# Performance work log

Hardware: AMD Instinct MI355X
Metric: run time of the kernel (lower is better)

The kernel has to match this reference:

```python
import jax, jax.numpy as jnp
import numpy as np
import math

N_HEADS = 16
D_MODEL = 1024
DK = D_MODEL // N_HEADS
B, S = 2, 2048


def setup_inputs() -> dict:
    key = jax.random.key(0)
    ks = jax.random.split(key, 11)
    scale_in = 1.0 / math.sqrt(D_MODEL)
    scale_o = 1.0 / math.sqrt(N_HEADS * DK)
    return {
        "query": jax.random.normal(ks[0], (B, S, D_MODEL), jnp.float32),
        "key": jax.random.normal(ks[1], (B, S, D_MODEL), jnp.float32),
        "value": jax.random.normal(ks[2], (B, S, D_MODEL), jnp.float32),
        # stacked per-head projection weights [H, d_model, dk], biases [H, dk]
        "Wq": jax.random.normal(ks[3], (N_HEADS, D_MODEL, DK), jnp.float32) * scale_in,
        "bq": jax.random.normal(ks[4], (N_HEADS, DK), jnp.float32) * scale_in,
        "Wk": jax.random.normal(ks[5], (N_HEADS, D_MODEL, DK), jnp.float32) * scale_in,
        "bk": jax.random.normal(ks[6], (N_HEADS, DK), jnp.float32) * scale_in,
        "Wv": jax.random.normal(ks[7], (N_HEADS, D_MODEL, DK), jnp.float32) * scale_in,
        "bv": jax.random.normal(ks[8], (N_HEADS, DK), jnp.float32) * scale_in,
        "Wo": jax.random.normal(ks[9], (N_HEADS * DK, D_MODEL), jnp.float32) * scale_o,
        "bo": jax.random.normal(ks[10], (D_MODEL,), jnp.float32) * scale_o,
    }


def reference(query, key, value, Wq, bq, Wk, bk, Wv, bv, Wo, bo):
    # Per-head linear projections, vectorized over heads: [B,H,S,dk]
    q = jnp.einsum("bsd,hdk->bhsk", query, Wq) + bq[None, :, None, :]
    k = jnp.einsum("bsd,hdk->bhsk", key, Wk) + bk[None, :, None, :]
    v = jnp.einsum("bsd,hdk->bhsk", value, Wv) + bv[None, :, None, :]
    # Scaled dot-product scores [B,H,S,S]
    scores = jnp.einsum("bhsk,bhtk->bhst", q, k) / jnp.sqrt(jnp.asarray(DK, q.dtype))
    # FAITHFUL to source: nn.Softmax(dim=0) -> softmax over the BATCH axis
    attn = jax.nn.softmax(scores, axis=0)
    out = jnp.einsum("bhst,bhtk->bhsk", attn, v)  # [B,H,S,dk]
    # concat heads along feature dim (torch.cat dim=2)
    concat = out.transpose(0, 2, 1, 3).reshape(query.shape[0], query.shape[1], N_HEADS * DK)
    return concat @ Wo + bo
```

## Files before the change

kernel.cpp:

```cpp
#include <hip/hip_runtime.h>
#include <hip/hip_bf16.h>

#define B_ 2
#define S_ 2048
#define D_ 1024
#define H_ 16
#define DK_ 64
#define BS_ (B_ * S_)

typedef unsigned int u32;
typedef unsigned short u16;
typedef __attribute__((ext_vector_type(8))) short bf16x8;
typedef __attribute__((ext_vector_type(4))) float f32x4;

typedef const __attribute__((address_space(1))) void glb_cv;
typedef __attribute__((address_space(3))) void lds_v;

__device__ __forceinline__ void async_cp16(const void* g, void* l) {
    __builtin_amdgcn_global_load_lds((glb_cv*)g, (lds_v*)l, 16, 0, 0);
}

__device__ __forceinline__ float bf2f(u16 v) {
    union { u32 u; float f; } c; c.u = ((u32)v) << 16; return c.f;
}
__device__ __forceinline__ u16 f2bf(float f) {
    union { float f; u32 u; } c; c.f = f;
    u32 u = c.u;
    return (u16)((u + 0x7fffu + ((u >> 16) & 1u)) >> 16);
}
__device__ __forceinline__ u32 pack2(float a, float b) {
    return (u32)f2bf(a) | ((u32)f2bf(b) << 16);
}
__device__ __forceinline__ u32 packtr(float lo, float hi) {
    union { float f; u32 u; } a, b; a.f = lo; b.f = hi;
    return __builtin_amdgcn_perm(b.u, a.u, 0x07060302u);
}
__device__ __forceinline__ int sw64(int r, int c8) { return (((c8) + (r)) & 7) * 8; }

struct PrepArgs {
    const float* W[4]; u16* WT[4];
    const float* X[3]; u16* XB[3];
};
__global__ __launch_bounds__(256) void prep(PrepArgs a)
{
    const int id = blockIdx.x;
    const int tid = threadIdx.x;
    if (id >= 1024) {
        const int cid = id - 1024;
        const int z = cid >> 11;
        const size_t base = (size_t)(cid & 2047) * 2048 + tid * 8;
        const float* X = a.X[z];
        float4 x0 = *(const float4*)(X + base);
        float4 x1 = *(const float4*)(X + base + 4);
        uint4 o;
        o.x = pack2(x0.x, x0.y); o.y = pack2(x0.z, x0.w);
        o.z = pack2(x1.x, x1.y); o.w = pack2(x1.z, x1.w);
        *(uint4*)(a.XB[z] + base) = o;
        return;
    }
    __shared__ __attribute__((aligned(16))) u16 T[64][72];
    const int z = id >> 8;
    const int rem = id & 255;
    const float* W = a.W[z];
    u16* WT = a.WT[z];
    const int headMode = (z < 3) ? 1 : 0;
    const int k0 = (rem >> 4) * 64;
    const int n0 = (rem & 15) * 64;
    const int kr = tid >> 4;
    const int n4 = (tid & 15) * 4;
    #pragma unroll
    for (int pass = 0; pass < 4; ++pass) {
        int kk = k0 + pass * 16 + kr;
        const float* p = headMode
            ? (W + (size_t)((n0 + n4) >> 6) * (1024 * 64) + kk * 64 + ((n0 + n4) & 63))
            : (W + (size_t)kk * 1024 + n0 + n4);
        float4 v = *(const float4*)p;
        int krel = pass * 16 + kr;
        T[n4 + 0][krel] = f2bf(v.x);
        T[n4 + 1][krel] = f2bf(v.y);
        T[n4 + 2][krel] = f2bf(v.z);
        T[n4 + 3][krel] = f2bf(v.w);
    }
    __syncthreads();
    const int nr = tid >> 2;
    const int kq = (tid & 3) * 16;
    uint4 o0 = *(const uint4*)&T[nr][kq];
    uint4 o1 = *(const uint4*)&T[nr][kq + 8];
    u16* q = WT + (size_t)(n0 + nr) * 1024 + k0 + kq;
    *(uint4*)q = o0;
    *(uint4*)(q + 8) = o1;
}

struct ProjArgs {
    const u16* X[3];
    const u16* W[3];
    const float* bias[3];
    u16* Y[3];
};
__global__ __launch_bounds__(256) void proj3(ProjArgs pa)
{
    __shared__ __attribute__((aligned(16))) u16 As[2][128][32];
    __shared__ __attribute__((aligned(16))) u16 Bs[2][128][32];
    const int z = blockIdx.z;
    const u16* X = pa.X[z];
    const u16* WT = pa.W[z];
    const float* bias = pa.bias[z];
    u16* Y = pa.Y[z];
    const int neg = (z == 1);

    const int tid = threadIdx.x;
    const int lane = tid & 63;
    const int wave = tid >> 6;
    const int quad = lane >> 4;
    const int l16 = lane & 15;
    const int m0 = blockIdx.x * 128;
    const int n0 = blockIdx.y * 128;
    const int wm = (wave & 1) * 64, wn = (wave >> 1) * 64;

    f32x4 acc[4][4] = {};

    for (int k0 = 0; k0 < 1024; k0 += 64) {
        __syncthreads();
        #pragma unroll
        for (int ks = 0; ks < 2; ++ks)
            #pragma unroll
            for (int call = 0; call < 2; ++call) {
                const int c = tid + call * 256;
                const int row = c >> 2, cc = (c & 3) * 8;
                char* la = (char*)&As[ks][0][0] + (size_t)(c & ~63) * 16;
                async_cp16(X + (size_t)(m0 + row) * 1024 + k0 + ks * 32 + cc, la);
                char* lb = (char*)&Bs[ks][0][0] + (size_t)(c & ~63) * 16;
                async_cp16(WT + (size_t)(n0 + row) * 1024 + k0 + ks * 32 + cc, lb);
            }
        __syncthreads();

        #pragma unroll
        for (int ks = 0; ks < 2; ++ks) {
            bf16x8 af[4], bfr[4];
            #pragma unroll
            for (int mt = 0; mt < 4; ++mt)
                af[mt] = *(const bf16x8*)&As[ks][wm + mt * 16 + l16][quad * 8];
            #pragma unroll
            for (int nt = 0; nt < 4; ++nt)
                bfr[nt] = *(const bf16x8*)&Bs[ks][wn + nt * 16 + l16][quad * 8];
            #pragma unroll
            for (int mt = 0; mt < 4; ++mt)
                #pragma unroll
                for (int nt = 0; nt < 4; ++nt)
                    acc[mt][nt] = __builtin_amdgcn_mfma_f32_16x16x32_bf16(
                        af[mt], bfr[nt], acc[mt][nt], 0, 0, 0);
        }
    }

    if (z == 2) {
        #pragma unroll
        for (int nt = 0; nt < 4; ++nt) {
            const int col = n0 + wn + nt * 16 + l16;
            const float bv = bias[col];
            u16* vrow = Y + ((size_t)(col >> 6) * 64 + (col & 63)) * 2048;
            #pragma unroll
            for (int mt = 0; mt < 4; ++mt) {
                const int row = m0 + wm + mt * 16 + quad * 4;
                const size_t boff = (size_t)(row >> 11) * (16 * 64 * 2048);
                const int t = row & 2047;
                uint2 w;
                w.x = pack2(acc[mt][nt][0] + bv, acc[mt][nt][1] + bv);
                w.y = pack2(acc[mt][nt][2] + bv, acc[mt][nt][3] + bv);
                *(uint2*)(vrow + boff + t) = w;
            }
        }
        return;
    }

    #pragma unroll
    for (int nt = 0; nt < 4; ++nt) {
        const int col = n0 + wn + nt * 16 + l16;
        const float bv = bias[col];
        #pragma unroll
        for (int mt = 0; mt < 4; ++mt) {
            #pragma unroll
            for (int r = 0; r < 4; ++r) {
                const int row = m0 + wm + mt * 16 + quad * 4 + r;
                float v = acc[mt][nt][r] + bv;
                if (neg && row >= 2048) v = -v;
                Y[(size_t)row * 1024 + col] = f2bf(v);
            }
        }
    }
}

__global__ __launch_bounds__(256) void gemm_out(
    const u16* __restrict__ P0, const u16* __restrict__ P1,
    const u16* __restrict__ P2, const float* __restrict__ csP,
    const u16* __restrict__ WT, const float* __restrict__ bias,
    float* __restrict__ Y)
{
    __shared__ __attribute__((aligned(16))) u16 Aa[128][32];
    __shared__ __attribute__((aligned(16))) u16 Ab[128][32];
    __shared__ __attribute__((aligned(16))) u16 Ac[128][32];
    __shared__ __attribute__((aligned(16))) u16 Bs[64][32];
    __shared__ __attribute__((aligned(16))) float csL[1024];

    const int tid = threadIdx.x;
    const int lane = tid & 63;
    const int wave = tid >> 6;
    const int quad = lane >> 4;
    const int l16 = lane & 15;
    const int m0 = blockIdx.x * 128;
    const int n0 = blockIdx.y * 64;
    const int wm = (wave & 1) * 64, wn = (wave >> 1) * 32;
    const bool hiB = (m0 >= 2048);

    {
        const int t4 = tid * 4;
        float4 c0 = *(const float4*)(csP + t4);
        float4 c1 = *(const float4*)(csP + 1024 + t4);
        float4 c2 = *(const float4*)(csP + 2048 + t4);
        csL[t4 + 0] = c0.x + c1.x + c2.x;
        csL[t4 + 1] = c0.y + c1.y + c2.y;
        csL[t4 + 2] = c0.z + c1.z + c2.z;
        csL[t4 + 3] = c0.w + c1.w + c2.w;
    }

    f32x4 acc[4][2] = {};

    for (int k0 = 0; k0 < 1024; k0 += 32) {
        __syncthreads();
        #pragma unroll
        for (int call = 0; call < 2; ++call) {
            const int c = tid + call * 256;
            const int row = c >> 2, cc = (c & 3) * 8;
            char* la = (char*)&Aa[0][0] + (size_t)(c & ~63) * 16;
            async_cp16(P0 + (size_t)(m0 + row) * 1024 + k0 + cc, la);
            char* lb = (char*)&Ab[0][0] + (size_t)(c & ~63) * 16;
            async_cp16(P1 + (size_t)(m0 + row) * 1024 + k0 + cc, lb);
            char* lc = (char*)&Ac[0][0] + (size_t)(c & ~63) * 16;
            async_cp16(P2 + (size_t)(m0 + row) * 1024 + k0 + cc, lc);
        }
        {
            const int c = tid;
            const int row = c >> 2, cc = (c & 3) * 8;
            char* lb = (char*)&Bs[0][0] + (size_t)(c & ~63) * 16;
            async_cp16(WT + (size_t)(n0 + row) * 1024 + k0 + cc, lb);
        }
        __syncthreads();

        float4 cs0, cs1;
        if (hiB) {
            cs0 = *(const float4*)&csL[k0 + quad * 8];
            cs1 = *(const float4*)&csL[k0 + quad * 8 + 4];
        }
        bf16x8 af[4], bfr[2];
        #pragma unroll
        for (int mt = 0; mt < 4; ++mt) {
            bf16x8 aa = *(const bf16x8*)&Aa[wm + mt * 16 + l16][quad * 8];
            bf16x8 ab = *(const bf16x8*)&Ab[wm + mt * 16 + l16][quad * 8];
            bf16x8 ac = *(const bf16x8*)&Ac[wm + mt * 16 + l16][quad * 8];
            float v[8];
            #pragma unroll
            for (int jj = 0; jj < 8; ++jj)
                v[jj] = bf2f((u16)aa[jj]) + bf2f((u16)ab[jj]) + bf2f((u16)ac[jj]);
            if (hiB) {
                v[0] = cs0.x - v[0]; v[1] = cs0.y - v[1];
                v[2] = cs0.z - v[2]; v[3] = cs0.w - v[3];
                v[4] = cs1.x - v[4]; v[5] = cs1.y - v[5];
                v[6] = cs1.z - v[6]; v[7] = cs1.w - v[7];
            }
            u32* rp = (u32*)&af[mt];
            rp[0] = pack2(v[0], v[1]); rp[1] = pack2(v[2], v[3]);
            rp[2] = pack2(v[4], v[5]); rp[3] = pack2(v[6], v[7]);
        }
        #pragma unroll
        for (int nt = 0; nt < 2; ++nt)
            bfr[nt] = *(const bf16x8*)&Bs[wn + nt * 16 + l16][quad * 8];
        #pragma unroll
        for (int mt = 0; mt < 4; ++mt)
            #pragma unroll
            for (int nt = 0; nt < 2; ++nt)
                acc[mt][nt] = __builtin_amdgcn_mfma_f32_16x16x32_bf16(
                    af[mt], bfr[nt], acc[mt][nt], 0, 0, 0);
    }

    #pragma unroll
    for (int nt = 0; nt < 2; ++nt) {
        const int col = n0 + wn + nt * 16 + l16;
        const float bv = bias[col];
        #pragma unroll
        for (int mt = 0; mt < 4; ++mt) {
            #pragma unroll
            for (int r = 0; r < 4; ++r) {
                const int row = m0 + wm + mt * 16 + quad * 4 + r;
                Y[(size_t)row * 1024 + col] = acc[mt][nt][r] + bv;
            }
        }
    }
}

__global__ __launch_bounds__(256, 3) void attn_mfma(
    const u16* __restrict__ Qb, const u16* __restrict__ Kb,
    const u16* __restrict__ VT, float* __restrict__ csP,
    u16* __restrict__ P0, u16* __restrict__ P1, u16* __restrict__ P2)
{
    __shared__ __attribute__((aligned(16))) u16 Ks[2][64][64];
    __shared__ __attribute__((aligned(16))) u16 Vs[2][64][64];
    __shared__ __attribute__((aligned(16))) u16 Ps[128][64];

    const int id = blockIdx.x;
    const int xcd = id & 7;
    const int j = id >> 3;
    const int h = xcd * 2 + (j & 1);
    const int r = j >> 1;
    const int st = r & 15;
    const int spl = r >> 4;
    const int s0 = st * 128;
    const int tstart = spl * 704;
    const int ntile = (spl == 2) ? 10 : 11;
    u16* Pout = (spl == 0) ? P0 : (spl == 1) ? P1 : P2;

    const int tid = threadIdx.x;
    const int lane = tid & 63;
    const int wave = tid >> 6;
    const int quad = lane >> 4;
    const int l16 = lane & 15;
    const int sr8 = lane >> 3;
    const int sc8 = lane & 7;

    auto stageK = [&](int t0) {
        #pragma unroll
        for (int c = 0; c < 4; ++c) {
            const int kc = c * 4 + wave;
            const int bb = kc >> 3, row0 = (kc & 7) * 8;
            const int rr = row0 + sr8;
            const int cg = (sc8 - rr) & 7;
            async_cp16(Kb + (size_t)(bb * S_ + t0 + rr) * 1024 + h * 64 + cg * 8,
                       &Ks[bb][row0][0]);
        }
    };
    auto stageV = [&](int t0) {
        #pragma unroll
        for (int c = 0; c < 4; ++c) {
            const int kc = c * 4 + wave;
            const int bb = kc >> 3, row0 = (kc & 7) * 8;
            const int rr = row0 + sr8;
            const int cg = (sc8 - rr) & 7;
            async_cp16(VT + ((size_t)(bb * H_ + h) * 64 + rr) * 2048 + t0 + cg * 8,
                       &Vs[bb][row0][0]);
        }
    };

    bf16x8 qf[2][2][2];
    #pragma unroll
    for (int sg = 0; sg < 2; ++sg)
        #pragma unroll
        for (int b = 0; b < 2; ++b)
            #pragma unroll
            for (int ks = 0; ks < 2; ++ks)
                qf[sg][b][ks] = *(const bf16x8*)(Qb
                    + (size_t)(b * S_ + s0 + wave * 32 + sg * 16 + l16) * 1024
                    + h * 64 + ks * 32 + quad * 8);

    f32x4 O0[2][4] = {}, T1[2][4] = {};
    float cacc = 0.f;

    stageK(tstart);
    __syncthreads();
    for (int i = 0; i < ntile; ++i) {
        const int t0 = tstart + i * 64;
        stageV(t0);

        f32x4 dacc[2][4] = {};
        __builtin_amdgcn_s_setprio(1);
        #pragma unroll
        for (int mt = 0; mt < 4; ++mt) {
            const int kr = mt * 16 + l16;
            #pragma unroll
            for (int ks = 0; ks < 2; ++ks) {
                bf16x8 k0f = *(const bf16x8*)&Ks[0][kr][sw64(kr, ks * 4 + quad)];
                bf16x8 k1f = *(const bf16x8*)&Ks[1][kr][sw64(kr, ks * 4 + quad)];
                #pragma unroll
                for (int sg = 0; sg < 2; ++sg) {
                    dacc[sg][mt] = __builtin_amdgcn_mfma_f32_16x16x32_bf16(
                        k0f, qf[sg][0][ks], dacc[sg][mt], 0, 0, 0);
                    dacc[sg][mt] = __builtin_amdgcn_mfma_f32_16x16x32_bf16(
                        k1f, qf[sg][1][ks], dacc[sg][mt], 0, 0, 0);
                }
            }
        }
        __builtin_amdgcn_s_setprio(0);

        #pragma unroll
        for (int sg = 0; sg < 2; ++sg) {
            const int pr = wave * 32 + sg * 16 + l16;
            #pragma unroll
            for (int mt = 0; mt < 4; ++mt) {
                float p[4];
                #pragma unroll
                for (int rr = 0; rr < 4; ++rr) {
                    float e = __expf(dacc[sg][mt][rr] * -0.125f);
                    p[rr] = __builtin_amdgcn_rcpf(1.0f + e);
                }
                uint2 w;
                w.x = packtr(p[0], p[1]);
                w.y = packtr(p[2], p[3]);
                const int c8 = 2 * mt + (quad >> 1);
                *(uint2*)&Ps[pr][sw64(pr, c8) + (quad & 1) * 4] = w;
            }
        }

        __syncthreads();

        if (i + 1 < ntile) stageK(t0 + 64);

        if (st == 0) {
            const int dk = tid >> 2, tp = tid & 3;
            bf16x8 vA = *(const bf16x8*)&Vs[1][dk][sw64(dk, tp * 2)];
            bf16x8 vB = *(const bf16x8*)&Vs[1][dk][sw64(dk, tp * 2 + 1)];
            #pragma unroll
            for (int jj = 0; jj < 8; ++jj)
                cacc += bf2f((u16)vA[jj]) + bf2f((u16)vB[jj]);
        }

        bf16x8 pf[2][2];
        #pragma unroll
        for (int sg = 0; sg < 2; ++sg) {
            const int pr = wave * 32 + sg * 16 + l16;
            pf[sg][0] = *(const bf16x8*)&Ps[pr][sw64(pr, quad)];
            pf[sg][1] = *(const bf16x8*)&Ps[pr][sw64(pr, 4 + quad)];
        }
        __builtin_amdgcn_s_setprio(1);
        #pragma unroll
        for (int nt = 0; nt < 4; ++nt) {
            const int vr = nt * 16 + l16;
            bf16x8 v00 = *(const bf16x8*)&Vs[0][vr][sw64(vr, quad)];
            bf16x8 v01 = *(const bf16x8*)&Vs[0][vr][sw64(vr, 4 + quad)];
            bf16x8 v10 = *(const bf16x8*)&Vs[1][vr][sw64(vr, quad)];
            bf16x8 v11 = *(const bf16x8*)&Vs[1][vr][sw64(vr, 4 + quad)];
            #pragma unroll
            for (int sg = 0; sg < 2; ++sg) {
                O0[sg][nt] = __builtin_amdgcn_mfma_f32_16x16x32_bf16(pf[sg][0], v00, O0[sg][nt], 0, 0, 0);
                O0[sg][nt] = __builtin_amdgcn_mfma_f32_16x16x32_bf16(pf[sg][1], v01, O0[sg][nt], 0, 0, 0);
                T1[sg][nt] = __builtin_amdgcn_mfma_f32_16x16x32_bf16(pf[sg][0], v10, T1[sg][nt], 0, 0, 0);
                T1[sg][nt] = __builtin_amdgcn_mfma_f32_16x16x32_bf16(pf[sg][1], v11, T1[sg][nt], 0, 0, 0);
            }
        }
        __builtin_amdgcn_s_setprio(0);
        __syncthreads();
    }

    #pragma unroll
    for (int sg = 0; sg < 2; ++sg)
        #pragma unroll
        for (int nt = 0; nt < 4; ++nt) {
            const int dk = nt * 16 + l16;
            #pragma unroll
            for (int rr = 0; rr < 4; ++rr) {
                const int s = s0 + wave * 32 + sg * 16 + quad * 4 + rr;
                Pout[(size_t)(0 * S_ + s) * 1024 + h * 64 + dk] = f2bf(O0[sg][nt][rr]);
                Pout[(size_t)(1 * S_ + s) * 1024 + h * 64 + dk] = f2bf(T1[sg][nt][rr]);
            }
        }

    if (st == 0) {
        cacc += __shfl_xor(cacc, 1);
        cacc += __shfl_xor(cacc, 2);
        if ((tid & 3) == 0)
            csP[spl * 1024 + h * 64 + (tid >> 2)] = cacc;
    }
}

extern "C" void kernel_launch(void* const* d_in, const int* in_sizes, int n_in,
                              void* d_out, int out_size, void* d_ws, size_t ws_size,
                              hipStream_t stream) {
    const float* q  = (const float*)d_in[0];
    const float* k  = (const float*)d_in[1];
    const float* v  = (const float*)d_in[2];
    const float* Wq = (const float*)d_in[3];
    const float* bq = (const float*)d_in[4];
    const float* Wk = (const float*)d_in[5];
    const float* bk = (const float*)d_in[6];
    const float* Wv = (const float*)d_in[7];
    const float* bv = (const float*)d_in[8];
    const float* Wo = (const float*)d_in[9];
    const float* bo = (const float*)d_in[10];

    char* ws = (char*)d_ws;
    const size_t MB = 1024 * 1024;
    u16* Xq  = (u16*)(ws);
    u16* Pa  = (u16*)(ws);
    u16* WqT = (u16*)(ws + 8  * MB);
    float* csP = (float*)(ws + 8 * MB);
    u16* WkT = (u16*)(ws + 10 * MB);
    u16* WvT = (u16*)(ws + 12 * MB);
    u16* WoT = (u16*)(ws + 14 * MB);
    u16* Qp  = (u16*)(ws + 16 * MB);
    u16* Kp  = (u16*)(ws + 24 * MB);
    u16* VTv = (u16*)(ws + 32 * MB);
    u16* Xk  = (u16*)(ws + 40 * MB);
    u16* Pb  = (u16*)(ws + 40 * MB);
    u16* Xv  = (u16*)(ws + 48 * MB);
    u16* Pc  = (u16*)(ws + 48 * MB);

    dim3 blk(256);

    PrepArgs pr;
    pr.W[0] = Wq; pr.W[1] = Wk; pr.W[2] = Wv; pr.W[3] = Wo;
    pr.WT[0] = WqT; pr.WT[1] = WkT; pr.WT[2] = WvT; pr.WT[3] = WoT;
    pr.X[0] = q; pr.X[1] = k; pr.X[2] = v;
    pr.XB[0] = Xq; pr.XB[1] = Xk; pr.XB[2] = Xv;
    prep<<<dim3(1024 + 6144), blk, 0, stream>>>(pr);

    ProjArgs pa;
    pa.X[0] = Xq; pa.X[1] = Xk; pa.X[2] = Xv;
    pa.W[0] = WqT; pa.W[1] = WkT; pa.W[2] = WvT;
    pa.bias[0] = bq; pa.bias[1] = bk; pa.bias[2] = bv;
    pa.Y[0] = Qp; pa.Y[1] = Kp; pa.Y[2] = VTv;
    proj3<<<dim3(32, 8, 3), blk, 0, stream>>>(pa);

    attn_mfma<<<dim3(768), blk, 0, stream>>>(Qp, Kp, VTv, csP, Pa, Pb, Pc);
    gemm_out<<<dim3(32, 16), blk, 0, stream>>>(Pa, Pb, Pc, csP, WoT, bo, (float*)d_out);
}
```

Before: 256.6 us.

## Replace per-element A-sum/complement conversion with three MFMAs and rank-1 column correction

The output GEMM used to add three bf16 partial-P tiles in fp32 and, for the second batch half, subtract them from a column-sum vector before repacking to bf16. It now issues three MFMAs, one per partial tile, straight from LDS data. For the second batch it computes a per-output-column dot product of the column sum with Wo and applies cs·W − acc in the epilogue. This removes the bf16→fp32→bf16 conversion VALU work from the inner loop but triples MFMA count, and it changes rounding because the sum is no longer rounded to bf16 before the multiply.

```diff
diff --git a/kernel.cpp b/kernel.cpp
--- a/kernel.cpp
+++ b/kernel.cpp
@@ -200,6 +200,7 @@
     __shared__ __attribute__((aligned(16))) u16 Ac[128][32];
     __shared__ __attribute__((aligned(16))) u16 Bs[64][32];
     __shared__ __attribute__((aligned(16))) float csL[1024];
+    __shared__ float csRowL[64];
 
     const int tid = threadIdx.x;
     const int lane = tid & 63;
@@ -211,7 +212,7 @@
     const int wm = (wave & 1) * 64, wn = (wave >> 1) * 32;
     const bool hiB = (m0 >= 2048);
 
-    {
+    if (hiB) {
         const int t4 = tid * 4;
         float4 c0 = *(const float4*)(csP + t4);
         float4 c1 = *(const float4*)(csP + 1024 + t4);
@@ -221,6 +222,10 @@
         csL[t4 + 2] = c0.z + c1.z + c2.z;
         csL[t4 + 3] = c0.w + c1.w + c2.w;
     }
+
+    const int ccol = tid >> 2;
+    const int ckq = (tid & 3) * 8;
+    float csAcc = 0.f;
 
     f32x4 acc[4][2] = {};
 
@@ -245,52 +250,56 @@
         }
         __syncthreads();
 
-        float4 cs0, cs1;
         if (hiB) {
-            cs0 = *(const float4*)&csL[k0 + quad * 8];
-            cs1 = *(const float4*)&csL[k0 + quad * 8 + 4];
-        }
-        bf16x8 af[4], bfr[2];
+            bf16x8 bv8 = *(const bf16x8*)&Bs[ccol][ckq];
+            float4 cl0 = *(const float4*)&csL[k0 + ckq];
+            float4 cl1 = *(const float4*)&csL[k0 + ckq + 4];
+            csAcc += cl0.x * bf2f((u16)bv8[0]) + cl0.y * bf2f((u16)bv8[1])
+                   + cl0.z * bf2f((u16)bv8[2]) + cl0.w * bf2f((u16)bv8[3])
+                   + cl1.x * bf2f((u16)bv8[4]) + cl1.y * bf2f((u16)bv8[5])
+                   + cl1.z * bf2f((u16)bv8[6]) + cl1.w * bf2f((u16)bv8[7]);
+        }
+
+        bf16x8 bfr[2];
+        #pragma unroll
+        for (int nt = 0; nt < 2; ++nt)
+            bfr[nt] = *(const bf16x8*)&Bs[wn + nt * 16 + l16][quad * 8];
         #pragma unroll
         for (int mt = 0; mt < 4; ++mt) {
             bf16x8 aa = *(const bf16x8*)&Aa[wm + mt * 16 + l16][quad * 8];
             bf16x8 ab = *(const bf16x8*)&Ab[wm + mt * 16 + l16][quad * 8];
             bf16x8 ac = *(const bf16x8*)&Ac[wm + mt * 16 + l16][quad * 8];
-            float v[8];
-            #pragma unroll
-            for (int jj = 0; jj < 8; ++jj)
-                v[jj] = bf2f((u16)aa[jj]) + bf2f((u16)ab[jj]) + bf2f((u16)ac[jj]);
-            if (hiB) {
-                v[0] = cs0.x - v[0]; v[1] = cs0.y - v[1];
-                v[2] = cs0.z - v[2]; v[3] = cs0.w - v[3];
-                v[4] = cs1.x - v[4]; v[5] = cs1.y - v[5];
-                v[6] = cs1.z - v[6]; v[7] = cs1.w - v[7];
-            }
-            u32* rp = (u32*)&af[mt];
-            rp[0] = pack2(v[0], v[1]); rp[1] = pack2(v[2], v[3]);
-            rp[2] = pack2(v[4], v[5]); rp[3] = pack2(v[6], v[7]);
-        }
-        #pragma unroll
-        for (int nt = 0; nt < 2; ++nt)
-            bfr[nt] = *(const bf16x8*)&Bs[wn + nt * 16 + l16][quad * 8];
-        #pragma unroll
-        for (int mt = 0; mt < 4; ++mt)
-            #pragma unroll
-            for (int nt = 0; nt < 2; ++nt)
+            #pragma unroll
+            for (int nt = 0; nt < 2; ++nt) {
                 acc[mt][nt] = __builtin_amdgcn_mfma_f32_16x16x32_bf16(
-                    af[mt], bfr[nt], acc[mt][nt], 0, 0, 0);
-    }
+                    aa, bfr[nt], acc[mt][nt], 0, 0, 0);
+                acc[mt][nt] = __builtin_amdgcn_mfma_f32_16x16x32_bf16(
+                    ab, bfr[nt], acc[mt][nt], 0, 0, 0);
+                acc[mt][nt] = __builtin_amdgcn_mfma_f32_16x16x32_bf16(
+                    ac, bfr[nt], acc[mt][nt], 0, 0, 0);
+            }
+        }
+    }
+
+    if (hiB) {
+        csAcc += __shfl_xor(csAcc, 1);
+        csAcc += __shfl_xor(csAcc, 2);
+        if ((tid & 3) == 0) csRowL[ccol] = csAcc;
+    }
+    __syncthreads();
 
     #pragma unroll
     for (int nt = 0; nt < 2; ++nt) {
         const int col = n0 + wn + nt * 16 + l16;
         const float bv = bias[col];
+        const float cr = hiB ? csRowL[wn + nt * 16 + l16] : 0.f;
         #pragma unroll
         for (int mt = 0; mt < 4; ++mt) {
             #pragma unroll
             for (int r = 0; r < 4; ++r) {
                 const int row = m0 + wm + mt * 16 + quad * 4 + r;
-                Y[(size_t)row * 1024 + col] = acc[mt][nt][r] + bv;
+                const float o = acc[mt][nt][r];
+                Y[(size_t)row * 1024 + col] = hiB ? (bv + cr - o) : (bv + o);
             }
         }
     }
```

After: 241.1 us. -6.1%, faster.
